# Kernel optimization log

Hardware: AMD Instinct MI355X
Metric: run time of the kernel (lower is better)

## Reference

```python
import jax, jax.numpy as jnp
import numpy as np

PATCH_LEN = 25
RATIO = 0.1
B, C, T = 128, 128, 5000
NUM_PATCHES = T // PATCH_LEN          # 200
TOTAL_UNITS = C * NUM_PATCHES         # 25600
NUM_MASK = int(TOTAL_UNITS * RATIO)   # 2560


def setup_inputs() -> dict:
    key = jax.random.key(0)
    kx, kp = jax.random.split(key)
    x = jax.random.normal(kx, (B, C, T), dtype=jnp.float32)
    # torch.randperm(total_units)[:num_mask] -> unique unit indices
    idx = jax.random.permutation(kp, TOTAL_UNITS)[:NUM_MASK].astype(jnp.int32)
    return {"x": x, "idx": idx}


def reference(x, idx):
    # Fused mask-generate-and-multiply: one scatter + one elementwise multiply
    # instead of num_mask separate slice-assign kernels.
    Bx, Cx, Tx = x.shape
    num_patches = Tx // PATCH_LEN
    # unit mask over (C * num_patches): 0 at masked units, 1 elsewhere
    unit_mask = jnp.ones((Cx * num_patches,), dtype=x.dtype).at[idx].set(0.0)
    # expand each unit to its patch_len samples -> (C, T)
    mask = jnp.repeat(unit_mask.reshape(Cx, num_patches), PATCH_LEN, axis=1)
    return x * mask[None, :, :]
```

## Files before the change

kernel.cpp:

```cpp
#include <hip/hip_runtime.h>


#define PM_B 128
#define PM_C 128
#define PM_T 5000
#define PM_PATCH 25
#define PM_NP 200
#define PM_UNITS (PM_C * PM_NP)
#define PM_NMASK 2560
#define PM_F4_PER_ROW (PM_T / 4)
#define PM_F4_TOTAL (PM_B * PM_C * PM_F4_PER_ROW)
#define PM_MWORDS (PM_UNITS / 32)

typedef float f32x4 __attribute__((ext_vector_type(4)));

__device__ __forceinline__ void pm_process(
    unsigned i, const f32x4* __restrict__ x, f32x4* __restrict__ out,
    const unsigned* mbits)
{
    const unsigned row = i / PM_F4_PER_ROW;
    const unsigned t0  = (i - row * PM_F4_PER_ROW) * 4u;
    const unsigned cbase = (row & (PM_C - 1)) * PM_NP;

    f32x4 v = __builtin_nontemporal_load(x + i);

    const unsigned p0 = t0 / PM_PATCH;
    const unsigned p3 = (t0 + 3u) / PM_PATCH;
    const unsigned u0 = cbase + p0;
    const float m0 = ((mbits[u0 >> 5] >> (u0 & 31u)) & 1u) ? 0.0f : 1.0f;
    if (p0 == p3) {
        v *= m0;
    } else {
        const unsigned u3 = cbase + p3;
        const float m3 = ((mbits[u3 >> 5] >> (u3 & 31u)) & 1u) ? 0.0f : 1.0f;
        const unsigned boundary = p3 * PM_PATCH;
        v.x *= (t0 + 0u < boundary) ? m0 : m3;
        v.y *= (t0 + 1u < boundary) ? m0 : m3;
        v.z *= (t0 + 2u < boundary) ? m0 : m3;
        v.w *= (t0 + 3u < boundary) ? m0 : m3;
    }

    __builtin_nontemporal_store(v, out + i);
}

__global__ __launch_bounds__(256) void pm_fused(
    const f32x4* __restrict__ x,
    const int* __restrict__ idx,
    f32x4* __restrict__ out)
{
    __shared__ unsigned mbits[PM_MWORDS];

    for (unsigned w = threadIdx.x; w < PM_MWORDS; w += 256u)
        mbits[w] = 0u;
    __syncthreads();
    for (unsigned j = threadIdx.x; j < PM_NMASK; j += 256u) {
        const unsigned u = (unsigned)idx[j];
        atomicOr(&mbits[u >> 5], 1u << (u & 31u));
    }
    __syncthreads();

    unsigned i = blockIdx.x * 256u + threadIdx.x;
    const unsigned stride = gridDim.x * 256u;
    for (; i + stride < PM_F4_TOTAL; i += 2u * stride) {
        pm_process(i,          x, out, mbits);
        pm_process(i + stride, x, out, mbits);
    }
    if (i < PM_F4_TOTAL)
        pm_process(i, x, out, mbits);
}

extern "C" void kernel_launch(void* const* d_in, const int* in_sizes, int n_in,
                              void* d_out, int out_size, void* d_ws, size_t ws_size,
                              hipStream_t stream) {
    const float* x   = (const float*)d_in[0];
    const int*   idx = (const int*)d_in[1];
    float*       out = (float*)d_out;

    pm_fused<<<2048, 256, 0, stream>>>(
        (const f32x4*)x, idx, (f32x4*)out);
}
```

Measured before the change: 123.8 us.

## Split mask bitset build into separate kernel and process 8 floats per thread

Builds the mask bitset once in a single-block kernel writing to the workspace, instead of having every one of 2048 blocks rebuild it in shared memory with atomics. The apply kernel then reads the bitset from global memory (cached) and handles 8 floats per iteration via two 16-byte loads. This removes redundant per-block setup and two barriers, but adds a second kernel launch and global-memory mask lookups in place of LDS reads.

```diff
diff --git a/kernel.cpp b/kernel.cpp
--- a/kernel.cpp
+++ b/kernel.cpp
@@ -8,65 +8,65 @@
 #define PM_NP 200
 #define PM_UNITS (PM_C * PM_NP)
 #define PM_NMASK 2560
-#define PM_F4_PER_ROW (PM_T / 4)
-#define PM_F4_TOTAL (PM_B * PM_C * PM_F4_PER_ROW)
 #define PM_MWORDS (PM_UNITS / 32)
+#define PM_F8_PER_ROW (PM_T / 8)
+#define PM_F8_TOTAL (PM_B * PM_C * PM_F8_PER_ROW)
 
 typedef float f32x4 __attribute__((ext_vector_type(4)));
 
-__device__ __forceinline__ void pm_process(
-    unsigned i, const f32x4* __restrict__ x, f32x4* __restrict__ out,
-    const unsigned* mbits)
+__global__ __launch_bounds__(256) void pm_build_bits(
+    const int* __restrict__ idx, unsigned* __restrict__ mbits)
 {
-    const unsigned row = i / PM_F4_PER_ROW;
-    const unsigned t0  = (i - row * PM_F4_PER_ROW) * 4u;
-    const unsigned cbase = (row & (PM_C - 1)) * PM_NP;
-
-    f32x4 v = __builtin_nontemporal_load(x + i);
-
-    const unsigned p0 = t0 / PM_PATCH;
-    const unsigned p3 = (t0 + 3u) / PM_PATCH;
-    const unsigned u0 = cbase + p0;
-    const float m0 = ((mbits[u0 >> 5] >> (u0 & 31u)) & 1u) ? 0.0f : 1.0f;
-    if (p0 == p3) {
-        v *= m0;
-    } else {
-        const unsigned u3 = cbase + p3;
-        const float m3 = ((mbits[u3 >> 5] >> (u3 & 31u)) & 1u) ? 0.0f : 1.0f;
-        const unsigned boundary = p3 * PM_PATCH;
-        v.x *= (t0 + 0u < boundary) ? m0 : m3;
-        v.y *= (t0 + 1u < boundary) ? m0 : m3;
-        v.z *= (t0 + 2u < boundary) ? m0 : m3;
-        v.w *= (t0 + 3u < boundary) ? m0 : m3;
-    }
-
-    __builtin_nontemporal_store(v, out + i);
-}
-
-__global__ __launch_bounds__(256) void pm_fused(
-    const f32x4* __restrict__ x,
-    const int* __restrict__ idx,
-    f32x4* __restrict__ out)
-{
-    __shared__ unsigned mbits[PM_MWORDS];
-
-    for (unsigned w = threadIdx.x; w < PM_MWORDS; w += 256u)
-        mbits[w] = 0u;
+    const unsigned tid = threadIdx.x;
+    uint4 z = {0u, 0u, 0u, 0u};
+    for (unsigned w = tid; w < PM_MWORDS / 4; w += 256u)
+        ((uint4*)mbits)[w] = z;
     __syncthreads();
-    for (unsigned j = threadIdx.x; j < PM_NMASK; j += 256u) {
+    for (unsigned j = tid; j < PM_NMASK; j += 256u) {
         const unsigned u = (unsigned)idx[j];
         atomicOr(&mbits[u >> 5], 1u << (u & 31u));
     }
-    __syncthreads();
+}
 
-    unsigned i = blockIdx.x * 256u + threadIdx.x;
+__global__ __launch_bounds__(256) void pm_apply_mask(
+    const f32x4* __restrict__ x,
+    const unsigned* __restrict__ mbits,
+    f32x4* __restrict__ out)
+{
+    unsigned k = blockIdx.x * 256u + threadIdx.x;
     const unsigned stride = gridDim.x * 256u;
-    for (; i + stride < PM_F4_TOTAL; i += 2u * stride) {
-        pm_process(i,          x, out, mbits);
-        pm_process(i + stride, x, out, mbits);
+    for (; k < PM_F8_TOTAL; k += stride) {
+        const unsigned row = k / PM_F8_PER_ROW;
+        const unsigned t0  = (k - row * PM_F8_PER_ROW) * 8u;
+        const unsigned cbase = (row & (PM_C - 1)) * PM_NP;
+
+        f32x4 v0 = __builtin_nontemporal_load(x + 2u * k);
+        f32x4 v1 = __builtin_nontemporal_load(x + 2u * k + 1u);
+
+        const unsigned p0 = t0 / PM_PATCH;
+        const unsigned p7 = (t0 + 7u) / PM_PATCH;
+        const unsigned u0 = cbase + p0;
+        const float m0 = ((mbits[u0 >> 5] >> (u0 & 31u)) & 1u) ? 0.0f : 1.0f;
+        if (p0 == p7) {
+            v0 *= m0;
+            v1 *= m0;
+        } else {
+            const unsigned u7 = cbase + p7;
+            const float m7 = ((mbits[u7 >> 5] >> (u7 & 31u)) & 1u) ? 0.0f : 1.0f;
+            const unsigned boundary = p7 * PM_PATCH;
+            v0.x *= (t0 + 0u < boundary) ? m0 : m7;
+            v0.y *= (t0 + 1u < boundary) ? m0 : m7;
+            v0.z *= (t0 + 2u < boundary) ? m0 : m7;
+            v0.w *= (t0 + 3u < boundary) ? m0 : m7;
+            v1.x *= (t0 + 4u < boundary) ? m0 : m7;
+            v1.y *= (t0 + 5u < boundary) ? m0 : m7;
+            v1.z *= (t0 + 6u < boundary) ? m0 : m7;
+            v1.w *= (t0 + 7u < boundary) ? m0 : m7;
+        }
+
+        __builtin_nontemporal_store(v0, out + 2u * k);
+        __builtin_nontemporal_store(v1, out + 2u * k + 1u);
     }
-    if (i < PM_F4_TOTAL)
-        pm_process(i, x, out, mbits);
 }
 
 extern "C" void kernel_launch(void* const* d_in, const int* in_sizes, int n_in,
@@ -75,7 +75,10 @@
     const float* x   = (const float*)d_in[0];
     const int*   idx = (const int*)d_in[1];
     float*       out = (float*)d_out;
+    unsigned*    mb  = (unsigned*)d_ws;
 
-    pm_fused<<<2048, 256, 0, stream>>>(
-        (const f32x4*)x, idx, (f32x4*)out);
+    pm_build_bits<<<1, 256, 0, stream>>>(idx, mb);
+
+    pm_apply_mask<<<2048, 256, 0, stream>>>(
+        (const f32x4*)x, mb, (f32x4*)out);
 }
```

New measurement: 148.2 us. +19.7%, slower.
